# Kernel tuning notes

Hardware: AMD Instinct MI355X
Metric: run time of the kernel (lower is better)

The kernel has to match this reference:

```python
import jax, jax.numpy as jnp
import numpy as np

DIM_IN = 256
HIDDEN = 32
NUM_EXPERTS = 64
N_TOKENS = 1048576
TEMP = 0.1
TOPK = 2


def setup_inputs() -> dict:
    key = jax.random.key(0)
    k_x, k_w1, k_b1, k_w2, k_b2 = jax.random.split(key, 5)
    s1 = 1.0 / np.sqrt(DIM_IN)
    s2 = 1.0 / np.sqrt(HIDDEN)
    return {
        "x": jax.random.normal(k_x, (N_TOKENS, DIM_IN), dtype=jnp.float32),
        "W1": jax.random.uniform(k_w1, (DIM_IN, HIDDEN), dtype=jnp.float32, minval=-s1, maxval=s1),
        "b1": jax.random.uniform(k_b1, (HIDDEN,), dtype=jnp.float32, minval=-s1, maxval=s1),
        "W2": jax.random.uniform(k_w2, (HIDDEN, NUM_EXPERTS), dtype=jnp.float32, minval=-s2, maxval=s2),
        "b2": jax.random.uniform(k_b2, (NUM_EXPERTS,), dtype=jnp.float32, minval=-s2, maxval=s2),
    }


def reference(x, W1, b1, W2, b2):
    # tiny 2-layer MLP router: [N, dim_in] -> [N, E]
    h = jnp.tanh(x @ W1 + b1)
    logits = h @ W2 + b2
    p_soft = jax.nn.softmax(logits / TEMP, axis=-1)

    # top-k mask + renormalize (no-grad branch in torch)
    p_ng = jax.lax.stop_gradient(p_soft)
    _, topk_idx = jax.lax.top_k(p_ng, TOPK)                 # [N, k]
    mask = jax.nn.one_hot(topk_idx, NUM_EXPERTS, dtype=p_soft.dtype).sum(axis=1)  # [N, E]
    p_hard = p_ng * mask
    p_hard = p_hard / (p_hard.sum(axis=-1, keepdims=True) + 1e-9)

    # straight-through combine: forward = p_hard, backward = p_soft
    w = p_soft + jax.lax.stop_gradient(p_hard - p_soft)
    return w
```

## Files before the change

kernel.cpp:

```cpp
#include <hip/hip_runtime.h>
#include <cfloat>

#define DIM_IN 256
#define HIDDEN 32
#define NE 64
#define ECH 16
#define BLOCK 256

__launch_bounds__(BLOCK, 4)
__global__ void router_fwd(const float* __restrict__ x,
                           const float* __restrict__ W1,
                           const float* __restrict__ b1,
                           const float* __restrict__ W2,
                           const float* __restrict__ b2,
                           float* __restrict__ out, int n) {
  __shared__ float obuf[BLOCK][ECH + 1];
  const int tid = threadIdx.x;
  const int t   = blockIdx.x * BLOCK + tid;
  const bool active = t < n;

  const float4* __restrict__ xr =
      reinterpret_cast<const float4*>(x + (size_t)(active ? t : 0) * DIM_IN);

  float h[HIDDEN];
#pragma unroll
  for (int j = 0; j < HIDDEN; ++j) h[j] = 0.0f;

#pragma unroll 1
  for (int i0 = 0; i0 < DIM_IN; i0 += 16) {
    const float4 x0 = xr[(i0 >> 2) + 0];
    const float4 x1 = xr[(i0 >> 2) + 1];
    const float4 x2 = xr[(i0 >> 2) + 2];
    const float4 x3 = xr[(i0 >> 2) + 3];
    const float xs[16] = {x0.x, x0.y, x0.z, x0.w, x1.x, x1.y, x1.z, x1.w,
                          x2.x, x2.y, x2.z, x2.w, x3.x, x3.y, x3.z, x3.w};
#pragma unroll
    for (int k = 0; k < 16; ++k) {
      const float* __restrict__ wrow = W1 + (i0 + k) * HIDDEN;
      const float xv = xs[k];
#pragma unroll
      for (int j = 0; j < HIDDEN; ++j) h[j] = fmaf(xv, wrow[j], h[j]);
    }
  }

#pragma unroll
  for (int j = 0; j < HIDDEN; ++j) {
    const float v = h[j] + b1[j];
    const float e = __expf(2.0f * v);
    h[j] = 1.0f - 2.0f / (e + 1.0f);
  }

  float v1 = -FLT_MAX, v2 = -FLT_MAX, S = 0.0f;
  int   i1 = 0, i2 = 0;

#pragma unroll 1
  for (int c = 0; c < NE / ECH; ++c) {
    float zc[ECH];
#pragma unroll
    for (int e = 0; e < ECH; ++e) zc[e] = 0.0f;
#pragma unroll
    for (int j = 0; j < HIDDEN; ++j) {
      const float hv = h[j];
      const float* __restrict__ wrow = W2 + j * NE + c * ECH;
#pragma unroll
      for (int e = 0; e < ECH; ++e) zc[e] = fmaf(hv, wrow[e], zc[e]);
    }
    const float m_prev = v1;
#pragma unroll
    for (int e = 0; e < ECH; ++e) {
      const float v = (zc[e] + b2[c * ECH + e]) * 10.0f;
      zc[e] = v;
      const int ge = c * ECH + e;
      const bool g1 = v > v1;
      const bool g2 = v > v2;
      v2 = g1 ? v1 : (g2 ? v : v2);
      i2 = g1 ? i1 : (g2 ? ge : i2);
      v1 = g1 ? v : v1;
      i1 = g1 ? ge : i1;
    }
    S *= __expf(m_prev - v1);
#pragma unroll
    for (int e = 0; e < ECH; ++e) S += __expf(zc[e] - v1);
  }

  const float pa = 1.0f / S;
  const float pb = __expf(v2 - v1) / S;
  const float d  = pa + pb + 1e-9f;
  const float oa = active ? pa / d : 0.0f;
  const float ob = active ? pb / d : 0.0f;

  const long obase = (long)blockIdx.x * BLOCK;
#pragma unroll 1
  for (int c = 0; c < NE / ECH; ++c) {
    __syncthreads();
#pragma unroll
    for (int e = 0; e < ECH; ++e) {
      const int ge = c * ECH + e;
      obuf[tid][e] = (ge == i1) ? oa : ((ge == i2) ? ob : 0.0f);
    }
    __syncthreads();
#pragma unroll
    for (int m = 0; m < 4; ++m) {
      const int f = m * BLOCK + tid;
      const int tok = f >> 2, part = f & 3;
      if (obase + tok < n) {
        float4 v;
        v.x = obuf[tok][part * 4 + 0];
        v.y = obuf[tok][part * 4 + 1];
        v.z = obuf[tok][part * 4 + 2];
        v.w = obuf[tok][part * 4 + 3];
        reinterpret_cast<float4*>(out + (obase + tok) * (long)NE + c * ECH)[part] = v;
      }
    }
  }
}

extern "C" void kernel_launch(void* const* d_in, const int* in_sizes, int n_in,
                              void* d_out, int out_size, void* d_ws, size_t ws_size,
                              hipStream_t stream) {
  const float* x  = (const float*)d_in[0];
  const float* W1 = (const float*)d_in[1];
  const float* b1 = (const float*)d_in[2];
  const float* W2 = (const float*)d_in[3];
  const float* b2 = (const float*)d_in[4];
  float* out = (float*)d_out;
  const int n_tokens = in_sizes[0] / DIM_IN;
  const int grid = (n_tokens + BLOCK - 1) / BLOCK;
  hipLaunchKernelGGL(router_fwd, dim3(grid), dim3(BLOCK), 0, stream,
                     x, W1, b1, W2, b2, out, n_tokens);
}
```

Before: 378.4 us.

## Process two tokens per thread with prefetched x loads and nontemporal stores

Each thread now computes two tokens, so every W1/W2 weight load (scalar, likely SGPR/constant loads) feeds two FMAs instead of one. The x-row loads are software-pipelined, with the next 8 floats prefetched while the current ones are consumed. Output writes use nontemporal stores to keep the write stream out of the cache. The cost is doubled accumulator registers (64 for h), which may reduce occupancy under launch_bounds(256,4) or cause spills, and the grid is halved.

```diff
diff --git a/kernel.cpp b/kernel.cpp
--- a/kernel.cpp
+++ b/kernel.cpp
@@ -6,6 +6,9 @@
 #define NE 64
 #define ECH 16
 #define BLOCK 256
+#define TPT 2
+
+typedef float f32x4 __attribute__((ext_vector_type(4)));
 
 __launch_bounds__(BLOCK, 4)
 __global__ void router_fwd(const float* __restrict__ x,
@@ -16,100 +19,154 @@
                            float* __restrict__ out, int n) {
   __shared__ float obuf[BLOCK][ECH + 1];
   const int tid = threadIdx.x;
-  const int t   = blockIdx.x * BLOCK + tid;
-  const bool active = t < n;
+  const long base = (long)blockIdx.x * (BLOCK * TPT);
+  const long t0 = base + tid;
+  const long t1 = base + BLOCK + tid;
+  const bool av0 = t0 < n, av1 = t1 < n;
 
-  const float4* __restrict__ xr =
-      reinterpret_cast<const float4*>(x + (size_t)(active ? t : 0) * DIM_IN);
+  const float4* __restrict__ xr0 =
+      reinterpret_cast<const float4*>(x + (av0 ? t0 : 0) * DIM_IN);
+  const float4* __restrict__ xr1 =
+      reinterpret_cast<const float4*>(x + (av1 ? t1 : 0) * DIM_IN);
 
-  float h[HIDDEN];
+  float h0[HIDDEN], h1[HIDDEN];
 #pragma unroll
-  for (int j = 0; j < HIDDEN; ++j) h[j] = 0.0f;
+  for (int j = 0; j < HIDDEN; ++j) h0[j] = h1[j] = 0.0f;
+
+  float4 c00 = xr0[0], c01 = xr0[1];
+  float4 c10 = xr1[0], c11 = xr1[1];
 
 #pragma unroll 1
-  for (int i0 = 0; i0 < DIM_IN; i0 += 16) {
-    const float4 x0 = xr[(i0 >> 2) + 0];
-    const float4 x1 = xr[(i0 >> 2) + 1];
-    const float4 x2 = xr[(i0 >> 2) + 2];
-    const float4 x3 = xr[(i0 >> 2) + 3];
-    const float xs[16] = {x0.x, x0.y, x0.z, x0.w, x1.x, x1.y, x1.z, x1.w,
-                          x2.x, x2.y, x2.z, x2.w, x3.x, x3.y, x3.z, x3.w};
+  for (int i0 = 0; i0 < DIM_IN - 8; i0 += 8) {
+    const float4 n00 = xr0[(i0 >> 2) + 2], n01 = xr0[(i0 >> 2) + 3];
+    const float4 n10 = xr1[(i0 >> 2) + 2], n11 = xr1[(i0 >> 2) + 3];
+    const float xs0[8] = {c00.x, c00.y, c00.z, c00.w, c01.x, c01.y, c01.z, c01.w};
+    const float xs1[8] = {c10.x, c10.y, c10.z, c10.w, c11.x, c11.y, c11.z, c11.w};
 #pragma unroll
-    for (int k = 0; k < 16; ++k) {
+    for (int k = 0; k < 8; ++k) {
       const float* __restrict__ wrow = W1 + (i0 + k) * HIDDEN;
-      const float xv = xs[k];
 #pragma unroll
-      for (int j = 0; j < HIDDEN; ++j) h[j] = fmaf(xv, wrow[j], h[j]);
+      for (int j = 0; j < HIDDEN; ++j) {
+        const float w = wrow[j];
+        h0[j] = fmaf(xs0[k], w, h0[j]);
+        h1[j] = fmaf(xs1[k], w, h1[j]);
+      }
+    }
+    c00 = n00; c01 = n01; c10 = n10; c11 = n11;
+  }
+  {
+    const int i0 = DIM_IN - 8;
+    const float xs0[8] = {c00.x, c00.y, c00.z, c00.w, c01.x, c01.y, c01.z, c01.w};
+    const float xs1[8] = {c10.x, c10.y, c10.z, c10.w, c11.x, c11.y, c11.z, c11.w};
+#pragma unroll
+    for (int k = 0; k < 8; ++k) {
+      const float* __restrict__ wrow = W1 + (i0 + k) * HIDDEN;
+#pragma unroll
+      for (int j = 0; j < HIDDEN; ++j) {
+        const float w = wrow[j];
+        h0[j] = fmaf(xs0[k], w, h0[j]);
+        h1[j] = fmaf(xs1[k], w, h1[j]);
+      }
     }
   }
 
 #pragma unroll
   for (int j = 0; j < HIDDEN; ++j) {
-    const float v = h[j] + b1[j];
-    const float e = __expf(2.0f * v);
-    h[j] = 1.0f - 2.0f / (e + 1.0f);
+    const float bj = b1[j];
+    const float e0 = __expf(2.0f * (h0[j] + bj));
+    const float e1 = __expf(2.0f * (h1[j] + bj));
+    h0[j] = 1.0f - 2.0f / (e0 + 1.0f);
+    h1[j] = 1.0f - 2.0f / (e1 + 1.0f);
   }
 
-  float v1 = -FLT_MAX, v2 = -FLT_MAX, S = 0.0f;
-  int   i1 = 0, i2 = 0;
+  float v1a = -FLT_MAX, v2a = -FLT_MAX, Sa = 0.0f;
+  float v1b = -FLT_MAX, v2b = -FLT_MAX, Sb = 0.0f;
+  int i1a = 0, i2a = 0, i1b = 0, i2b = 0;
 
 #pragma unroll 1
   for (int c = 0; c < NE / ECH; ++c) {
-    float zc[ECH];
+    float z0[ECH], z1[ECH];
 #pragma unroll
-    for (int e = 0; e < ECH; ++e) zc[e] = 0.0f;
+    for (int e = 0; e < ECH; ++e) z0[e] = z1[e] = 0.0f;
 #pragma unroll
     for (int j = 0; j < HIDDEN; ++j) {
-      const float hv = h[j];
       const float* __restrict__ wrow = W2 + j * NE + c * ECH;
+      const float ha = h0[j], hb = h1[j];
 #pragma unroll
-      for (int e = 0; e < ECH; ++e) zc[e] = fmaf(hv, wrow[e], zc[e]);
+      for (int e = 0; e < ECH; ++e) {
+        const float w = wrow[e];
+        z0[e] = fmaf(ha, w, z0[e]);
+        z1[e] = fmaf(hb, w, z1[e]);
+      }
     }
-    const float m_prev = v1;
+    const float ma = v1a, mb = v1b;
 #pragma unroll
     for (int e = 0; e < ECH; ++e) {
-      const float v = (zc[e] + b2[c * ECH + e]) * 10.0f;
-      zc[e] = v;
+      const float bz = b2[c * ECH + e];
       const int ge = c * ECH + e;
-      const bool g1 = v > v1;
-      const bool g2 = v > v2;
-      v2 = g1 ? v1 : (g2 ? v : v2);
-      i2 = g1 ? i1 : (g2 ? ge : i2);
-      v1 = g1 ? v : v1;
-      i1 = g1 ? ge : i1;
+      const float va = (z0[e] + bz) * 10.0f;
+      z0[e] = va;
+      bool g1 = va > v1a, g2 = va > v2a;
+      v2a = g1 ? v1a : (g2 ? va : v2a);
+      i2a = g1 ? i1a : (g2 ? ge : i2a);
+      v1a = g1 ? va : v1a;
+      i1a = g1 ? ge : i1a;
+      const float vb = (z1[e] + bz) * 10.0f;
+      z1[e] = vb;
+      g1 = vb > v1b; g2 = vb > v2b;
+      v2b = g1 ? v1b : (g2 ? vb : v2b);
+      i2b = g1 ? i1b : (g2 ? ge : i2b);
+      v1b = g1 ? vb : v1b;
+      i1b = g1 ? ge : i1b;
     }
-    S *= __expf(m_prev - v1);
+    Sa *= __expf(ma - v1a);
+    Sb *= __expf(mb - v1b);
 #pragma unroll
-    for (int e = 0; e < ECH; ++e) S += __expf(zc[e] - v1);
+    for (int e = 0; e < ECH; ++e) {
+      Sa += __expf(z0[e] - v1a);
+      Sb += __expf(z1[e] - v1b);
+    }
   }
 
-  const float pa = 1.0f / S;
-  const float pb = __expf(v2 - v1) / S;
-  const float d  = pa + pb + 1e-9f;
-  const float oa = active ? pa / d : 0.0f;
-  const float ob = active ? pb / d : 0.0f;
+  const float paA = 1.0f / Sa, pbA = __expf(v2a - v1a) / Sa;
+  const float dA = paA + pbA + 1e-9f;
+  const float oaA = av0 ? paA / dA : 0.0f;
+  const float obA = av0 ? pbA / dA : 0.0f;
+  const float paB = 1.0f / Sb, pbB = __expf(v2b - v1b) / Sb;
+  const float dB = paB + pbB + 1e-9f;
+  const float oaB = av1 ? paB / dB : 0.0f;
+  const float obB = av1 ? pbB / dB : 0.0f;
 
-  const long obase = (long)blockIdx.x * BLOCK;
 #pragma unroll 1
-  for (int c = 0; c < NE / ECH; ++c) {
-    __syncthreads();
+  for (int s = 0; s < TPT; ++s) {
+    const float oa = s == 0 ? oaA : oaB;
+    const float ob = s == 0 ? obA : obB;
+    const int i1 = s == 0 ? i1a : i1b;
+    const int i2 = s == 0 ? i2a : i2b;
+    const long sbase = base + (long)s * BLOCK;
+#pragma unroll 1
+    for (int c = 0; c < NE / ECH; ++c) {
+      __syncthreads();
 #pragma unroll
-    for (int e = 0; e < ECH; ++e) {
-      const int ge = c * ECH + e;
-      obuf[tid][e] = (ge == i1) ? oa : ((ge == i2) ? ob : 0.0f);
-    }
-    __syncthreads();
+      for (int e = 0; e < ECH; ++e) {
+        const int ge = c * ECH + e;
+        obuf[tid][e] = (ge == i1) ? oa : ((ge == i2) ? ob : 0.0f);
+      }
+      __syncthreads();
 #pragma unroll
-    for (int m = 0; m < 4; ++m) {
-      const int f = m * BLOCK + tid;
-      const int tok = f >> 2, part = f & 3;
-      if (obase + tok < n) {
-        float4 v;
-        v.x = obuf[tok][part * 4 + 0];
-        v.y = obuf[tok][part * 4 + 1];
-        v.z = obuf[tok][part * 4 + 2];
-        v.w = obuf[tok][part * 4 + 3];
-        reinterpret_cast<float4*>(out + (obase + tok) * (long)NE + c * ECH)[part] = v;
+      for (int m = 0; m < 4; ++m) {
+        const int f = m * BLOCK + tid;
+        const int tok = f >> 2, part = f & 3;
+        if (sbase + tok < n) {
+          f32x4 v;
+          v.x = obuf[tok][part * 4 + 0];
+          v.y = obuf[tok][part * 4 + 1];
+          v.z = obuf[tok][part * 4 + 2];
+          v.w = obuf[tok][part * 4 + 3];
+          f32x4* dst = reinterpret_cast<f32x4*>(
+              out + (sbase + tok) * (long)NE + c * ECH) + part;
+          __builtin_nontemporal_store(v, dst);
+        }
       }
     }
   }
@@ -125,7 +182,8 @@
   const float* b2 = (const float*)d_in[4];
   float* out = (float*)d_out;
   const int n_tokens = in_sizes[0] / DIM_IN;
-  const int grid = (n_tokens + BLOCK - 1) / BLOCK;
+  const int tokens_per_block = BLOCK * TPT;
+  const int grid = (n_tokens + tokens_per_block - 1) / tokens_per_block;
   hipLaunchKernelGGL(router_fwd, dim3(grid), dim3(BLOCK), 0, stream,
                      x, W1, b1, W2, b2, out, n_tokens);
 }
```

Measured after the change: 737.1 us. 94.8% more time.
